# Optimization experiments

Measured on AMD Instinct MI355X. Metric: run time of the kernel, lower is better.

The kernel has to match this reference:

```python
import jax, jax.numpy as jnp
import numpy as np

EMBED_DIM = 1024
HEAD_DIM = 64
B, T = 4, 4096


def setup_inputs() -> dict:
    key = jax.random.key(0)
    kx, kq, kk, kv = jax.random.split(key, 4)
    x = jax.random.normal(kx, (B, T, EMBED_DIM), dtype=jnp.float32)
    # nn.Linear weights, stored transposed as (in, out) for x @ W
    s = 1.0 / np.sqrt(EMBED_DIM)
    Wq = jax.random.normal(kq, (EMBED_DIM, HEAD_DIM), dtype=jnp.float32) * s
    Wk = jax.random.normal(kk, (EMBED_DIM, HEAD_DIM), dtype=jnp.float32) * s
    Wv = jax.random.normal(kv, (EMBED_DIM, HEAD_DIM), dtype=jnp.float32) * s
    return {"x": x, "Wq": Wq, "Wk": Wk, "Wv": Wv}


def reference(x, Wq, Wk, Wv):
    Bc, Tc, C = x.shape
    Q = x @ Wq  # [B, T, H]
    K = x @ Wk
    V = x @ Wv
    # NOTE: original scales by embedding_dim C, not head_dim
    scores = jnp.einsum('bqh,bkh->bqk', Q, K) / jnp.sqrt(jnp.float32(C))
    causal = jnp.tril(jnp.ones((Tc, Tc), dtype=bool))
    scores = jnp.where(causal, scores, -jnp.inf)
    attn = jax.nn.softmax(scores, axis=-1)
    return jnp.einsum('bqk,bkh->bqh', attn, V)
```

## Files before the change

### kernel.cpp

```cpp
#include <hip/hip_runtime.h>
#include <hip/hip_bf16.h>
#include <math.h>

typedef __attribute__((ext_vector_type(8))) short bf16x8;
typedef __attribute__((ext_vector_type(4))) float f32x4;

#define MFMA16 __builtin_amdgcn_mfma_f32_16x16x32_bf16

static constexpr int TSEQ = 4096;
static constexpr int EMB = 1024;
static constexpr int HD = 64;

__device__ __forceinline__ unsigned short f2bf(float f) {
    unsigned u = __builtin_bit_cast(unsigned, f);
    u += 0x7fffu + ((u >> 16) & 1u);
    return (unsigned short)(u >> 16);
}
__device__ __forceinline__ int pk2bf(float a, float b) {
    return (int)((unsigned)f2bf(a) | ((unsigned)f2bf(b) << 16));
}

union frag_u { int i[4]; bf16x8 v; };

__global__ void prep_w(const float* __restrict__ Wq, const float* __restrict__ Wk,
                       const float* __restrict__ Wv, unsigned short* __restrict__ Wp) {
    int id = blockIdx.x * 256 + threadIdx.x;
    int wsel = id >> 16;
    int t = id & 65535;
    int k = t >> 6, n0 = t & 63;
    const float* W = (wsel == 0) ? Wq : (wsel == 1) ? Wk : Wv;
    float v = W[t];
    if (wsel == 0) v *= 0.03125f;
    int n = wsel * 64 + n0;
    Wp[(k >> 5) * 6144 + n * 32 + (k & 31)] = f2bf(v);
}

__global__ __launch_bounds__(256, 4) void proj_kernel(const float* __restrict__ X,
        const unsigned short* __restrict__ Wp, unsigned short* __restrict__ Qp,
        unsigned short* __restrict__ Kp, unsigned short* __restrict__ Vp) {
    __shared__ float cmb[3][64][52];
    const int lane = threadIdx.x & 63, wave = threadIdx.x >> 6;
    const int col = lane & 15, quad = lane >> 4;
    const int row0 = blockIdx.x * 16;
    const int fragoff = col * 64 + quad * 16;
    const int perm = (col * 4 + quad) * 4;

    f32x4 acc[12];
#pragma unroll
    for (int t = 0; t < 12; t++) acc[t] = (f32x4)(0.0f);

    const float* xb = X + (size_t)(row0 + (lane >> 2)) * EMB + wave * 256 + (lane & 3) * 8;
    const char* wB = (const char*)Wp + (size_t)wave * 8 * 12288 + fragoff;

    for (int kc = 0; kc < 8; kc++) {
        const float* xp = xb + kc * 32;
        const float4 a0 = *(const float4*)(xp);
        const float4 b0 = *(const float4*)(xp + 4);
        frag_u A;
        {
            int s0 = pk2bf(a0.x, a0.y), s1 = pk2bf(a0.z, a0.w);
            int s2 = pk2bf(b0.x, b0.y), s3 = pk2bf(b0.z, b0.w);
            A.i[0] = __builtin_amdgcn_ds_bpermute(perm, s0);
            A.i[1] = __builtin_amdgcn_ds_bpermute(perm, s1);
            A.i[2] = __builtin_amdgcn_ds_bpermute(perm, s2);
            A.i[3] = __builtin_amdgcn_ds_bpermute(perm, s3);
        }
        const char* wp = wB + kc * 12288;
#pragma unroll
        for (int t = 0; t < 12; t++) {
            const bf16x8 w = *(const bf16x8*)(wp + t * 1024);
            acc[t] = MFMA16(A.v, w, acc[t], 0, 0, 0);
        }
    }

    if (wave) {
#pragma unroll
        for (int t = 0; t < 12; t++)
            *(f32x4*)&cmb[wave - 1][lane][t * 4] = acc[t];
    }
    __syncthreads();
    if (wave == 0) {
#pragma unroll
        for (int s = 0; s < 3; s++)
#pragma unroll
            for (int t = 0; t < 12; t++)
                acc[t] += *(const f32x4*)&cmb[s][lane][t * 4];

        const int tile = row0 >> 4;
        const int c = row0 >> 5;
        const int j = (row0 >> 4) & 1;
#pragma unroll
        for (int t = 0; t < 4; t++)
#pragma unroll
            for (int r = 0; r < 4; r++)
                Qp[tile * 1024 + (t >> 1) * 512 + (quad * 4 + r) * 32 +
                   ((t & 1) * 2 + (col >> 3)) * 8 + (col & 7)] = f2bf(acc[t][r]);
#pragma unroll
        for (int tt = 0; tt < 4; tt++)
#pragma unroll
            for (int r = 0; r < 4; r++)
                Kp[((c * 2 + j) * 2 + (tt >> 1)) * 512 + (quad * 4 + r) * 32 +
                   ((tt & 1) * 2 + (col >> 3)) * 8 + (col & 7)] = f2bf(acc[tt + 4][r]);
#pragma unroll
        for (int t4 = 0; t4 < 4; t4++) {
            ushort4 pk;
            pk.x = f2bf(acc[t4 + 8][0]); pk.y = f2bf(acc[t4 + 8][1]);
            pk.z = f2bf(acc[t4 + 8][2]); pk.w = f2bf(acc[t4 + 8][3]);
            *(ushort4*)&Vp[c * 2048 + t4 * 512 + col * 32 + j * 16 + quad * 4] = pk;
        }
    }
}

__global__ __launch_bounds__(512, 4) void attn_kernel(const unsigned short* __restrict__ Qp,
        const unsigned short* __restrict__ Kp, const unsigned short* __restrict__ Vp,
        float* __restrict__ Out) {
    __shared__ float cmb[4][2][64][20];
    __shared__ unsigned short plds[8][2][640];
    const int lane = threadIdx.x & 63, wave = threadIdx.x >> 6;
    const int col = lane & 15, quad = lane >> 4;
    const int batch = blockIdx.x & 3;
    const int ti = 127 - (blockIdx.x >> 2);
    const int q0 = ti * 32;
    const size_t bT = (size_t)batch * TSEQ;
    const int fragoff = col * 64 + quad * 16;

    const char* QpB = (const char*)Qp;
    const char* KpB = (const char*)Kp;
    const char* VpB = (const char*)Vp;
    const int gt = (int)((bT + q0) >> 4);
    const int c0 = (int)(bT >> 5);

    bf16x8 aq[2][2];
#pragma unroll
    for (int m = 0; m < 2; m++)
#pragma unroll
        for (int h = 0; h < 2; h++)
            aq[m][h] = *(const bf16x8*)(QpB + (size_t)((gt + m) * 2 + h) * 1024 + fragoff);

    f32x4 o[2][4];
    f32x4 lsum[2];
#pragma unroll
    for (int m = 0; m < 2; m++) {
        lsum[m] = (f32x4)(0.0f);
#pragma unroll
        for (int t = 0; t < 4; t++) o[m][t] = (f32x4)(0.0f);
    }

    for (int c = wave; c <= ti; c += 8) {
        const char* kb = KpB + (size_t)(c0 + c) * 4096;
        const char* vb = VpB + (size_t)(c0 + c) * 4096;
        bf16x8 bk[2][2], bv[4];
#pragma unroll
        for (int j = 0; j < 2; j++)
#pragma unroll
            for (int h = 0; h < 2; h++)
                bk[j][h] = *(const bf16x8*)(kb + j * 2048 + h * 1024 + fragoff);
#pragma unroll
        for (int t = 0; t < 4; t++)
            bv[t] = *(const bf16x8*)(vb + t * 1024 + fragoff);

        f32x4 s[2][2];
#pragma unroll
        for (int m = 0; m < 2; m++)
#pragma unroll
            for (int j = 0; j < 2; j++) {
                f32x4 a = MFMA16(aq[m][0], bk[j][0], (f32x4)(0.0f), 0, 0, 0);
                s[m][j] = MFMA16(aq[m][1], bk[j][1], a, 0, 0, 0);
            }
        const bool diag = (c == ti);
#pragma unroll
        for (int m = 0; m < 2; m++)
#pragma unroll
            for (int j = 0; j < 2; j++)
#pragma unroll
                for (int r = 0; r < 4; r++) {
                    float v = s[m][j][r];
                    if (diag && (j * 16 + col > m * 16 + quad * 4 + r)) v = -INFINITY;
                    const float p = __expf(v);
                    lsum[m][r] += p;
                    plds[wave][m][(quad * 4 + r) * 40 + j * 16 + col] =
                        (unsigned short)(__builtin_bit_cast(unsigned, p) >> 16);
                }
        bf16x8 pa[2];
#pragma unroll
        for (int m = 0; m < 2; m++)
            pa[m] = *(const bf16x8*)(&plds[wave][m][col * 40 + quad * 8]);
#pragma unroll
        for (int m = 0; m < 2; m++)
#pragma unroll
            for (int t = 0; t < 4; t++)
                o[m][t] = MFMA16(pa[m], bv[t], o[m][t], 0, 0, 0);
    }

    auto wr = [&](int s) {
#pragma unroll
        for (int m = 0; m < 2; m++) {
#pragma unroll
            for (int t = 0; t < 4; t++)
                *(f32x4*)&cmb[s][m][lane][t * 4] = o[m][t];
            *(f32x4*)&cmb[s][m][lane][16] = lsum[m];
        }
    };
    auto rd = [&](int s) {
#pragma unroll
        for (int m = 0; m < 2; m++) {
#pragma unroll
            for (int t = 0; t < 4; t++)
                o[m][t] += *(const f32x4*)&cmb[s][m][lane][t * 4];
            lsum[m] += *(const f32x4*)&cmb[s][m][lane][16];
        }
    };
    if (wave >= 4) wr(wave - 4);
    __syncthreads();
    if (wave < 4) rd(wave);
    __syncthreads();
    if (wave == 2 || wave == 3) wr(wave);
    __syncthreads();
    if (wave < 2) rd(wave + 2);
    __syncthreads();
    if (wave == 1) wr(1);
    __syncthreads();
    if (wave == 0) {
        rd(1);
#pragma unroll
        for (int off = 1; off < 16; off <<= 1)
#pragma unroll
            for (int m = 0; m < 2; m++)
#pragma unroll
                for (int r = 0; r < 4; r++)
                    lsum[m][r] += __shfl_xor(lsum[m][r], off, 64);
#pragma unroll
        for (int m = 0; m < 2; m++)
#pragma unroll
            for (int r = 0; r < 4; r++) {
                const float inv = 1.0f / lsum[m][r];
                const size_t orow = (bT + q0 + m * 16 + quad * 4 + r) * HD;
#pragma unroll
                for (int t = 0; t < 4; t++)
                    Out[orow + t * 16 + col] = o[m][t][r] * inv;
            }
    }
}

extern "C" void kernel_launch(void* const* d_in, const int* in_sizes, int n_in,
                              void* d_out, int out_size, void* d_ws, size_t ws_size,
                              hipStream_t stream) {
    const float* x  = (const float*)d_in[0];
    const float* Wq = (const float*)d_in[1];
    const float* Wk = (const float*)d_in[2];
    const float* Wv = (const float*)d_in[3];
    float* out = (float*)d_out;

    char* w = (char*)d_ws;
    unsigned short* Wp = (unsigned short*)(w);
    unsigned short* Qp = (unsigned short*)(w + (512 << 10));
    unsigned short* Kp = (unsigned short*)(w + (512 << 10) + (2 << 20));
    unsigned short* Vp = (unsigned short*)(w + (512 << 10) + (4 << 20));

    hipLaunchKernelGGL(prep_w, dim3(768), dim3(256), 0, stream, Wq, Wk, Wv, Wp);
    hipLaunchKernelGGL(proj_kernel, dim3(1024), dim3(256), 0, stream, x, Wp, Qp, Kp, Vp);
    hipLaunchKernelGGL(attn_kernel, dim3(512), dim3(512), 0, stream, Qp, Kp, Vp, out);
}
```

Baseline: 147.8 us.

## Restructure projection kernel: split output columns across waves, drop LDS K-reduction

The projection kernel now processes 32 rows per block and assigns each wave a 16-column slice of each of Q, K and V over the full K=1024 range, instead of splitting the reduction dimension across waves. This removes the LDS partial-sum combine, the barrier and the ds_bpermute shuffles. Each wave reuses its W fragments across two row tiles, and the X/W loads are software-prefetched one step ahead. The cost is a longer serial K loop per wave, since each wave now issues 32 iterations, and half as many blocks in the grid. Each X row is also read redundantly by all four waves.

```diff
diff --git a/kernel.cpp b/kernel.cpp
--- a/kernel.cpp
+++ b/kernel.cpp
@@ -35,79 +35,86 @@
     Wp[(k >> 5) * 6144 + n * 32 + (k & 31)] = f2bf(v);
 }
 
-__global__ __launch_bounds__(256, 4) void proj_kernel(const float* __restrict__ X,
+__global__ __launch_bounds__(256, 2) void proj_kernel(const float* __restrict__ X,
         const unsigned short* __restrict__ Wp, unsigned short* __restrict__ Qp,
         unsigned short* __restrict__ Kp, unsigned short* __restrict__ Vp) {
-    __shared__ float cmb[3][64][52];
     const int lane = threadIdx.x & 63, wave = threadIdx.x >> 6;
     const int col = lane & 15, quad = lane >> 4;
-    const int row0 = blockIdx.x * 16;
-    const int fragoff = col * 64 + quad * 16;
-    const int perm = (col * 4 + quad) * 4;
-
-    f32x4 acc[12];
-#pragma unroll
-    for (int t = 0; t < 12; t++) acc[t] = (f32x4)(0.0f);
-
-    const float* xb = X + (size_t)(row0 + (lane >> 2)) * EMB + wave * 256 + (lane & 3) * 8;
-    const char* wB = (const char*)Wp + (size_t)wave * 8 * 12288 + fragoff;
-
-    for (int kc = 0; kc < 8; kc++) {
-        const float* xp = xb + kc * 32;
-        const float4 a0 = *(const float4*)(xp);
-        const float4 b0 = *(const float4*)(xp + 4);
-        frag_u A;
-        {
-            int s0 = pk2bf(a0.x, a0.y), s1 = pk2bf(a0.z, a0.w);
-            int s2 = pk2bf(b0.x, b0.y), s3 = pk2bf(b0.z, b0.w);
-            A.i[0] = __builtin_amdgcn_ds_bpermute(perm, s0);
-            A.i[1] = __builtin_amdgcn_ds_bpermute(perm, s1);
-            A.i[2] = __builtin_amdgcn_ds_bpermute(perm, s2);
-            A.i[3] = __builtin_amdgcn_ds_bpermute(perm, s3);
-        }
-        const char* wp = wB + kc * 12288;
-#pragma unroll
-        for (int t = 0; t < 12; t++) {
-            const bf16x8 w = *(const bf16x8*)(wp + t * 1024);
-            acc[t] = MFMA16(A.v, w, acc[t], 0, 0, 0);
-        }
-    }
-
-    if (wave) {
-#pragma unroll
-        for (int t = 0; t < 12; t++)
-            *(f32x4*)&cmb[wave - 1][lane][t * 4] = acc[t];
-    }
-    __syncthreads();
-    if (wave == 0) {
-#pragma unroll
-        for (int s = 0; s < 3; s++)
-#pragma unroll
-            for (int t = 0; t < 12; t++)
-                acc[t] += *(const f32x4*)&cmb[s][lane][t * 4];
-
-        const int tile = row0 >> 4;
-        const int c = row0 >> 5;
-        const int j = (row0 >> 4) & 1;
-#pragma unroll
-        for (int t = 0; t < 4; t++)
-#pragma unroll
-            for (int r = 0; r < 4; r++)
-                Qp[tile * 1024 + (t >> 1) * 512 + (quad * 4 + r) * 32 +
-                   ((t & 1) * 2 + (col >> 3)) * 8 + (col & 7)] = f2bf(acc[t][r]);
-#pragma unroll
-        for (int tt = 0; tt < 4; tt++)
-#pragma unroll
-            for (int r = 0; r < 4; r++)
-                Kp[((c * 2 + j) * 2 + (tt >> 1)) * 512 + (quad * 4 + r) * 32 +
-                   ((tt & 1) * 2 + (col >> 3)) * 8 + (col & 7)] = f2bf(acc[tt + 4][r]);
-#pragma unroll
-        for (int t4 = 0; t4 < 4; t4++) {
-            ushort4 pk;
-            pk.x = f2bf(acc[t4 + 8][0]); pk.y = f2bf(acc[t4 + 8][1]);
-            pk.z = f2bf(acc[t4 + 8][2]); pk.w = f2bf(acc[t4 + 8][3]);
-            *(ushort4*)&Vp[c * 2048 + t4 * 512 + col * 32 + j * 16 + quad * 4] = pk;
-        }
+    const int row0 = blockIdx.x * 32;
+
+    f32x4 acc[2][3];
+#pragma unroll
+    for (int m = 0; m < 2; m++)
+#pragma unroll
+        for (int j = 0; j < 3; j++) acc[m][j] = (f32x4)(0.0f);
+
+    const float* xr0 = X + (size_t)(row0 + col) * EMB + quad * 8;
+    const float* xr1 = xr0 + 16 * EMB;
+    const char* wB = (const char*)Wp + wave * 1024 + col * 64 + quad * 16;
+
+    float4 xa[2][2];
+    bf16x8 wf[3];
+    xa[0][0] = *(const float4*)(xr0);
+    xa[0][1] = *(const float4*)(xr0 + 4);
+    xa[1][0] = *(const float4*)(xr1);
+    xa[1][1] = *(const float4*)(xr1 + 4);
+#pragma unroll
+    for (int j = 0; j < 3; j++) wf[j] = *(const bf16x8*)(wB + j * 4096);
+
+#pragma unroll 2
+    for (int kc = 0; kc < 32; kc++) {
+        float4 xn[2][2];
+        bf16x8 wn[3];
+        if (kc < 31) {
+            const float* p0 = xr0 + (kc + 1) * 32;
+            const float* p1 = xr1 + (kc + 1) * 32;
+            xn[0][0] = *(const float4*)(p0);
+            xn[0][1] = *(const float4*)(p0 + 4);
+            xn[1][0] = *(const float4*)(p1);
+            xn[1][1] = *(const float4*)(p1 + 4);
+            const char* wp = wB + (size_t)(kc + 1) * 12288;
+#pragma unroll
+            for (int j = 0; j < 3; j++) wn[j] = *(const bf16x8*)(wp + j * 4096);
+        }
+        frag_u A[2];
+#pragma unroll
+        for (int m = 0; m < 2; m++) {
+            A[m].i[0] = pk2bf(xa[m][0].x, xa[m][0].y);
+            A[m].i[1] = pk2bf(xa[m][0].z, xa[m][0].w);
+            A[m].i[2] = pk2bf(xa[m][1].x, xa[m][1].y);
+            A[m].i[3] = pk2bf(xa[m][1].z, xa[m][1].w);
+        }
+#pragma unroll
+        for (int m = 0; m < 2; m++)
+#pragma unroll
+            for (int j = 0; j < 3; j++)
+                acc[m][j] = MFMA16(A[m].v, wf[j], acc[m][j], 0, 0, 0);
+        if (kc < 31) {
+#pragma unroll
+            for (int m = 0; m < 2; m++)
+#pragma unroll
+                for (int h = 0; h < 2; h++) xa[m][h] = xn[m][h];
+#pragma unroll
+            for (int j = 0; j < 3; j++) wf[j] = wn[j];
+        }
+    }
+
+    const int tile0 = blockIdx.x * 2;
+    const int c = blockIdx.x;
+#pragma unroll
+    for (int m = 0; m < 2; m++) {
+#pragma unroll
+        for (int r = 0; r < 4; r++)
+            Qp[(tile0 + m) * 1024 + (wave >> 1) * 512 + (quad * 4 + r) * 32 +
+               ((wave & 1) * 2 + (col >> 3)) * 8 + (col & 7)] = f2bf(acc[m][0][r]);
+#pragma unroll
+        for (int r = 0; r < 4; r++)
+            Kp[((c * 2 + m) * 2 + (wave >> 1)) * 512 + (quad * 4 + r) * 32 +
+               ((wave & 1) * 2 + (col >> 3)) * 8 + (col & 7)] = f2bf(acc[m][1][r]);
+        ushort4 pk;
+        pk.x = f2bf(acc[m][2][0]); pk.y = f2bf(acc[m][2][1]);
+        pk.z = f2bf(acc[m][2][2]); pk.w = f2bf(acc[m][2][3]);
+        *(ushort4*)&Vp[c * 2048 + wave * 512 + col * 32 + m * 16 + quad * 4] = pk;
     }
 }
 
@@ -258,6 +265,6 @@
     unsigned short* Vp = (unsigned short*)(w + (512 << 10) + (4 << 20));
 
     hipLaunchKernelGGL(prep_w, dim3(768), dim3(256), 0, stream, Wq, Wk, Wv, Wp);
-    hipLaunchKernelGGL(proj_kernel, dim3(1024), dim3(256), 0, stream, x, Wp, Qp, Kp, Vp);
+    hipLaunchKernelGGL(proj_kernel, dim3(512), dim3(256), 0, stream, x, Wp, Qp, Kp, Vp);
     hipLaunchKernelGGL(attn_kernel, dim3(512), dim3(512), 0, stream, Qp, Kp, Vp, out);
 }
```

Measured after the change: 162.7 us. +10.1%, slower.

## Split projection by output columns across waves instead of K-split with LDS reduction

Applied to the files above, without the earlier changes.

The projection kernel previously split the K dimension across four waves, with each wave computing all 12 output tiles, then reduced through shared memory with a barrier. Now each wave owns 16 output columns each of Q, K and V (3 accumulators) and loops over the full K=1024 in 32 steps. Loads are software-pipelined with a 3-deep register prefetch of X and W fragments. The X fragment is loaded directly in MFMA layout, removing the ds_bpermute shuffles. This drops the LDS buffer, barrier and reduction, but every wave now reads the same X rows (four times the X traffic through cache) and runs a longer serial dependency chain per accumulator.

```diff
diff --git a/kernel.cpp b/kernel.cpp
--- a/kernel.cpp
+++ b/kernel.cpp
@@ -38,76 +38,65 @@
 __global__ __launch_bounds__(256, 4) void proj_kernel(const float* __restrict__ X,
         const unsigned short* __restrict__ Wp, unsigned short* __restrict__ Qp,
         unsigned short* __restrict__ Kp, unsigned short* __restrict__ Vp) {
-    __shared__ float cmb[3][64][52];
     const int lane = threadIdx.x & 63, wave = threadIdx.x >> 6;
     const int col = lane & 15, quad = lane >> 4;
     const int row0 = blockIdx.x * 16;
-    const int fragoff = col * 64 + quad * 16;
-    const int perm = (col * 4 + quad) * 4;
-
-    f32x4 acc[12];
-#pragma unroll
-    for (int t = 0; t < 12; t++) acc[t] = (f32x4)(0.0f);
-
-    const float* xb = X + (size_t)(row0 + (lane >> 2)) * EMB + wave * 256 + (lane & 3) * 8;
-    const char* wB = (const char*)Wp + (size_t)wave * 8 * 12288 + fragoff;
-
-    for (int kc = 0; kc < 8; kc++) {
-        const float* xp = xb + kc * 32;
-        const float4 a0 = *(const float4*)(xp);
-        const float4 b0 = *(const float4*)(xp + 4);
+
+    f32x4 acc[3];
+#pragma unroll
+    for (int j = 0; j < 3; j++) acc[j] = (f32x4)(0.0f);
+
+    const float* xr = X + (size_t)(row0 + col) * EMB + quad * 8;
+    const char* wB = (const char*)Wp + wave * 1024 + col * 64 + quad * 16;
+
+    float4 xa[3][2];
+    bf16x8 wf[3][3];
+#pragma unroll
+    for (int p = 0; p < 3; p++) {
+        const float* xp = xr + p * 32;
+        xa[p][0] = *(const float4*)(xp);
+        xa[p][1] = *(const float4*)(xp + 4);
+        const char* wp = wB + (size_t)p * 12288;
+#pragma unroll
+        for (int j = 0; j < 3; j++) wf[p][j] = *(const bf16x8*)(wp + j * 4096);
+    }
+
+#pragma unroll
+    for (int kc = 0; kc < 32; kc++) {
+        const int s = kc % 3;
         frag_u A;
-        {
-            int s0 = pk2bf(a0.x, a0.y), s1 = pk2bf(a0.z, a0.w);
-            int s2 = pk2bf(b0.x, b0.y), s3 = pk2bf(b0.z, b0.w);
-            A.i[0] = __builtin_amdgcn_ds_bpermute(perm, s0);
-            A.i[1] = __builtin_amdgcn_ds_bpermute(perm, s1);
-            A.i[2] = __builtin_amdgcn_ds_bpermute(perm, s2);
-            A.i[3] = __builtin_amdgcn_ds_bpermute(perm, s3);
+        A.i[0] = pk2bf(xa[s][0].x, xa[s][0].y);
+        A.i[1] = pk2bf(xa[s][0].z, xa[s][0].w);
+        A.i[2] = pk2bf(xa[s][1].x, xa[s][1].y);
+        A.i[3] = pk2bf(xa[s][1].z, xa[s][1].w);
+#pragma unroll
+        for (int j = 0; j < 3; j++)
+            acc[j] = MFMA16(A.v, wf[s][j], acc[j], 0, 0, 0);
+        if (kc + 3 < 32) {
+            const float* xp = xr + (kc + 3) * 32;
+            xa[s][0] = *(const float4*)(xp);
+            xa[s][1] = *(const float4*)(xp + 4);
+            const char* wp = wB + (size_t)(kc + 3) * 12288;
+#pragma unroll
+            for (int j = 0; j < 3; j++) wf[s][j] = *(const bf16x8*)(wp + j * 4096);
         }
-        const char* wp = wB + kc * 12288;
-#pragma unroll
-        for (int t = 0; t < 12; t++) {
-            const bf16x8 w = *(const bf16x8*)(wp + t * 1024);
-            acc[t] = MFMA16(A.v, w, acc[t], 0, 0, 0);
-        }
-    }
-
-    if (wave) {
-#pragma unroll
-        for (int t = 0; t < 12; t++)
-            *(f32x4*)&cmb[wave - 1][lane][t * 4] = acc[t];
-    }
-    __syncthreads();
-    if (wave == 0) {
-#pragma unroll
-        for (int s = 0; s < 3; s++)
-#pragma unroll
-            for (int t = 0; t < 12; t++)
-                acc[t] += *(const f32x4*)&cmb[s][lane][t * 4];
-
-        const int tile = row0 >> 4;
-        const int c = row0 >> 5;
-        const int j = (row0 >> 4) & 1;
-#pragma unroll
-        for (int t = 0; t < 4; t++)
-#pragma unroll
-            for (int r = 0; r < 4; r++)
-                Qp[tile * 1024 + (t >> 1) * 512 + (quad * 4 + r) * 32 +
-                   ((t & 1) * 2 + (col >> 3)) * 8 + (col & 7)] = f2bf(acc[t][r]);
-#pragma unroll
-        for (int tt = 0; tt < 4; tt++)
-#pragma unroll
-            for (int r = 0; r < 4; r++)
-                Kp[((c * 2 + j) * 2 + (tt >> 1)) * 512 + (quad * 4 + r) * 32 +
-                   ((tt & 1) * 2 + (col >> 3)) * 8 + (col & 7)] = f2bf(acc[tt + 4][r]);
-#pragma unroll
-        for (int t4 = 0; t4 < 4; t4++) {
-            ushort4 pk;
-            pk.x = f2bf(acc[t4 + 8][0]); pk.y = f2bf(acc[t4 + 8][1]);
-            pk.z = f2bf(acc[t4 + 8][2]); pk.w = f2bf(acc[t4 + 8][3]);
-            *(ushort4*)&Vp[c * 2048 + t4 * 512 + col * 32 + j * 16 + quad * 4] = pk;
-        }
+    }
+
+    const int tile = blockIdx.x;
+    const int c = tile >> 1, j2 = tile & 1;
+#pragma unroll
+    for (int r = 0; r < 4; r++)
+        Qp[tile * 1024 + (wave >> 1) * 512 + (quad * 4 + r) * 32 +
+           ((wave & 1) * 2 + (col >> 3)) * 8 + (col & 7)] = f2bf(acc[0][r]);
+#pragma unroll
+    for (int r = 0; r < 4; r++)
+        Kp[(tile * 2 + (wave >> 1)) * 512 + (quad * 4 + r) * 32 +
+           ((wave & 1) * 2 + (col >> 3)) * 8 + (col & 7)] = f2bf(acc[1][r]);
+    {
+        ushort4 pk;
+        pk.x = f2bf(acc[2][0]); pk.y = f2bf(acc[2][1]);
+        pk.z = f2bf(acc[2][2]); pk.w = f2bf(acc[2][3]);
+        *(ushort4*)&Vp[c * 2048 + wave * 512 + col * 32 + j2 * 16 + quad * 4] = pk;
     }
 }
 
```

Result: slower. 166.7 us (+12.8%).
